# Kernel tuning notes

Hardware: AMD Instinct MI355X
Metric: run time of the kernel (lower is better)

The kernel has to match this reference:

```python
import jax, jax.numpy as jnp
import numpy as np

B, T, S, E = 32, 256, 9, 631     # batch, time, index_len, emb_num
D, FF, H, L, OUT = 512, 512, 8, 2, 512  # d_model, ffn, heads, layers, output_dim
HD = D // H
EPS = 1e-5


def _layernorm(x, g, b):
    m = jnp.mean(x, axis=-1, keepdims=True)
    v = jnp.mean(jnp.square(x - m), axis=-1, keepdims=True)
    return (x - m) * jax.lax.rsqrt(v + EPS) * g + b


def _encoder_layer(h, qkv_w, qkv_b, out_w, out_b, ln1_g, ln1_b,
                   lin1_w, lin1_b, lin2_w, lin2_b, ln2_g, ln2_b):
    # h: (N, S, D). PyTorch post-norm TransformerEncoderLayer, relu activation, dropout=0.
    N = h.shape[0]
    qkv = h @ qkv_w + qkv_b                       # (N, S, 3D)
    q, k, v = jnp.split(qkv, 3, axis=-1)
    q = q.reshape(N, S, H, HD)
    k = k.reshape(N, S, H, HD)
    v = v.reshape(N, S, H, HD)
    scores = jnp.einsum('nqhd,nkhd->nhqk', q, k) / jnp.sqrt(jnp.float32(HD))
    attn = jax.nn.softmax(scores, axis=-1)
    ctx = jnp.einsum('nhqk,nkhd->nqhd', attn, v).reshape(N, S, D)
    h = _layernorm(h + (ctx @ out_w + out_b), ln1_g, ln1_b)
    ff = jax.nn.relu(h @ lin1_w + lin1_b) @ lin2_w + lin2_b
    return _layernorm(h + ff, ln2_g, ln2_b)


def _forward(x, adapt2_w, adapt2_b, adapt_w, adapt_b,
             qkv_w, qkv_b, out_w, out_b, ln1_g, ln1_b,
             lin1_w, lin1_b, lin2_w, lin2_b, ln2_g, ln2_b, fc_w, fc_b):
    # eye_mat[x] @ W^T is a row gather: adapt_layer(onehot) == adapt_w[x] + adapt_b
    emb = adapt_w[x] + adapt_b                               # (B, T, S, D)
    # adapt_ly2(onehot.reshape(B,T,9*E)) == sum_n W2r[n, x[...,n]] + b
    w2r = adapt2_w.reshape(S, E, OUT)
    raw_emb = w2r[jnp.arange(S)[None, None, :], x].sum(axis=2) + adapt2_b  # (B, T, OUT)

    h = emb.reshape(B * T, S, D)
    for l in range(L):
        h = _encoder_layer(h, qkv_w[l], qkv_b[l], out_w[l], out_b[l],
                           ln1_g[l], ln1_b[l], lin1_w[l], lin1_b[l],
                           lin2_w[l], lin2_b[l], ln2_g[l], ln2_b[l])
    cls = h[:, 0, :]                                         # x[0] in seq-first layout
    ov = (cls @ fc_w + fc_b).reshape(B, T, OUT)
    return raw_emb * (1.0 + jax.nn.relu(ov))


def setup_inputs() -> dict:
    key = jax.random.key(0)
    ks = jax.random.split(key, 20)
    s = 0.02
    inp = {
        'x': jax.random.randint(ks[0], (B, T, S), 0, E),
        'adapt2_w': jax.random.normal(ks[1], (S * E, OUT), jnp.float32) * s,
        'adapt2_b': jnp.zeros((OUT,), jnp.float32),
        'adapt_w': jax.random.normal(ks[2], (E, D), jnp.float32) * s,
        'adapt_b': jnp.zeros((D,), jnp.float32),
        'qkv_w': jax.random.normal(ks[3], (L, D, 3 * D), jnp.float32) * s,
        'qkv_b': jnp.zeros((L, 3 * D), jnp.float32),
        'out_w': jax.random.normal(ks[4], (L, D, D), jnp.float32) * s,
        'out_b': jnp.zeros((L, D), jnp.float32),
        'ln1_g': jnp.ones((L, D), jnp.float32),
        'ln1_b': jnp.zeros((L, D), jnp.float32),
        'lin1_w': jax.random.normal(ks[5], (L, D, FF), jnp.float32) * s,
        'lin1_b': jnp.zeros((L, FF), jnp.float32),
        'lin2_w': jax.random.normal(ks[6], (L, FF, D), jnp.float32) * s,
        'lin2_b': jnp.zeros((L, D), jnp.float32),
        'ln2_g': jnp.ones((L, D), jnp.float32),
        'ln2_b': jnp.zeros((L, D), jnp.float32),
        'fc_w': jax.random.normal(ks[7], (D, OUT), jnp.float32) * s,
        'fc_b': jnp.zeros((OUT,), jnp.float32),
    }
    return inp


def reference(x, adapt2_w, adapt2_b, adapt_w, adapt_b, qkv_w, qkv_b, out_w,
              out_b, ln1_g, ln1_b, lin1_w, lin1_b, lin2_w, lin2_b, ln2_g,
              ln2_b, fc_w, fc_b):
    return _forward(x, adapt2_w, adapt2_b, adapt_w, adapt_b, qkv_w, qkv_b,
                    out_w, out_b, ln1_g, ln1_b, lin1_w, lin1_b, lin2_w,
                    lin2_b, ln2_g, ln2_b, fc_w, fc_b)
```

## Files before the change

kernel.cpp:

```cpp
#include <hip/hip_runtime.h>
#include <hip/hip_bf16.h>
#include <stdint.h>

typedef __bf16 bf16;
typedef bf16 bf16x8 __attribute__((ext_vector_type(8)));
typedef bf16 bf16x2 __attribute__((ext_vector_type(2)));
typedef float f32x4 __attribute__((ext_vector_type(4)));

__device__ __forceinline__ float b2f(bf16 x) {
  unsigned short u = __builtin_bit_cast(unsigned short, x);
  unsigned int v = ((unsigned int)u) << 16;
  return __builtin_bit_cast(float, v);
}
__device__ __forceinline__ bf16 f2b(float f) {
  unsigned int u = __builtin_bit_cast(unsigned int, f);
  unsigned int r = (u + 0x7FFFu + ((u >> 16) & 1u)) >> 16;
  return __builtin_bit_cast(bf16, (unsigned short)r);
}

__device__ __forceinline__ void async_copy16(const bf16* g, bf16* l) {
  __builtin_amdgcn_global_load_lds(
      (const __attribute__((address_space(1))) void*)g,
      (__attribute__((address_space(3))) void*)l, 16, 0, 0);
}

template <int MFR, int LDA, int LDC, int RSTR, bool RELU, bool RESID, bool RAWG, bool F32OUT, bool SWZ>
__global__ __launch_bounds__(256, (MFR == 6 ? 2 : 4)) void gemm_kernel(
    const bf16* __restrict__ A,
    const bf16* __restrict__ BT,
    const float* __restrict__ bias,
    const bf16* __restrict__ resid,
    const float* __restrict__ rawg,
    bf16* __restrict__ Cb, float* __restrict__ Cf)
{
  constexpr int K = 512;
  constexpr int MROWS = MFR * 32;
  __shared__ bf16 As[MROWS * 64];
  __shared__ bf16 Bs[128 * 64];
  const int t = threadIdx.x;
  const int lane = t & 63;
  const int wave = t >> 6;

  int bx, by;
  if (SWZ) {
    const int gn = gridDim.x, gm = gridDim.y;
    int id = blockIdx.y * gn + blockIdx.x;
    int full = (gm & ~7) * gn;
    if (id < full) {
      int sg = id / (8 * gn);
      int r = id - sg * (8 * gn);
      by = sg * 8 + (r & 7);
      bx = r >> 3;
    } else {
      int r = id - full;
      int rem = gm - (gm & ~7);
      by = (gm & ~7) + (r % rem);
      bx = r / rem;
    }
  } else {
    bx = blockIdx.x; by = blockIdx.y;
  }

  const long m0 = (long)by * MROWS;
  const int n0 = bx * 128;
  const int wm = (wave >> 1) * (MFR * 16);
  const int wn = (wave & 1) * 64;
  const int row16 = lane & 15;
  const int quad = lane >> 4;

  f32x4 acc[MFR][4] = {};

  const bf16* gA[MFR]; const bf16* gB[4];
  bf16* lA[MFR]; bf16* lB[4];
#pragma unroll
  for (int i = 0; i < MFR; i++) {
    int c = i * 256 + t;
    int row = c >> 3;
    int kc = (c & 7) ^ (row & 7);
    gA[i] = A + (m0 + row) * LDA + kc * 8;
    lA[i] = As + i * 2048 + wave * 512;
  }
#pragma unroll
  for (int i = 0; i < 4; i++) {
    int c = i * 256 + t;
    int row = c >> 3;
    int kc = (c & 7) ^ (row & 7);
    gB[i] = BT + (long)(n0 + row) * K + kc * 8;
    lB[i] = Bs + i * 2048 + wave * 512;
  }

  const int rb7 = row16 & 7;
  const bf16* paA = As + (wm + row16) * 64;
  const bf16* pbB = Bs + (wn + row16) * 64;
  const int o0 = ((0 + quad) ^ rb7) * 8;
  const int o1 = ((4 + quad) ^ rb7) * 8;

#pragma unroll 1
  for (int kt = 0; kt < K; kt += 64) {
#pragma unroll
    for (int i = 0; i < MFR; i++) async_copy16(gA[i] + kt, lA[i]);
#pragma unroll
    for (int i = 0; i < 4; i++) async_copy16(gB[i] + kt, lB[i]);
    __syncthreads();
    {
      bf16x8 af[MFR], bfr[4];
#pragma unroll
      for (int i = 0; i < MFR; i++) af[i] = *(const bf16x8*)(paA + i * 1024 + o0);
#pragma unroll
      for (int i = 0; i < 4; i++) bfr[i] = *(const bf16x8*)(pbB + i * 1024 + o0);
#pragma unroll
      for (int mi = 0; mi < MFR; mi++)
#pragma unroll
        for (int ni = 0; ni < 4; ni++)
          acc[mi][ni] = __builtin_amdgcn_mfma_f32_16x16x32_bf16(af[mi], bfr[ni], acc[mi][ni], 0, 0, 0);
    }
    {
      bf16x8 af[MFR], bfr[4];
#pragma unroll
      for (int i = 0; i < MFR; i++) af[i] = *(const bf16x8*)(paA + i * 1024 + o1);
#pragma unroll
      for (int i = 0; i < 4; i++) bfr[i] = *(const bf16x8*)(pbB + i * 1024 + o1);
#pragma unroll
      for (int mi = 0; mi < MFR; mi++)
#pragma unroll
        for (int ni = 0; ni < 4; ni++)
          acc[mi][ni] = __builtin_amdgcn_mfma_f32_16x16x32_bf16(af[mi], bfr[ni], acc[mi][ni], 0, 0, 0);
    }
    __syncthreads();
  }

  float bv[4];
#pragma unroll
  for (int ni = 0; ni < 4; ni++) bv[ni] = bias[n0 + wn + ni * 16 + row16];
#pragma unroll
  for (int mi = 0; mi < MFR; mi++) {
    long rb = m0 + wm + mi * 16 + quad * 4;
#pragma unroll
    for (int ni = 0; ni < 4; ni++) {
      int col = n0 + wn + ni * 16 + row16;
#pragma unroll
      for (int r = 0; r < 4; r++) {
        float xv = acc[mi][ni][r] + bv[ni];
        if (RESID) xv += b2f(resid[(rb + r) * RSTR + col]);
        if (RELU) xv = fmaxf(xv, 0.f);
        if (RAWG) xv = rawg[(rb + r) * 512 + col] * (1.f + fmaxf(xv, 0.f));
        if (F32OUT) Cf[(rb + r) * LDC + col] = xv;
        else        Cb[(rb + r) * LDC + col] = f2b(xv);
      }
    }
  }
}

#define ROWP 520
__global__ __launch_bounds__(512) void attn_kernel(bf16* __restrict__ qkv)
{
  __shared__ bf16 q[9 * ROWP];
  __shared__ bf16 k[9 * ROWP];
  __shared__ bf16 v[9 * ROWP];
  __shared__ float sc[8 * 81];
  const long n = blockIdx.x;
  const int t = threadIdx.x;
  bf16* base = qkv + n * (9 * 1536);
  for (int c = t; c < 1728; c += 512) {
    int o = c * 8;
    int s = o / 1536;
    int col = o - s * 1536;
    bf16x8 rawv = *(const bf16x8*)(base + o);
    bf16* dst;
    int cc;
    if (col < 512)       { dst = q; cc = col; }
    else if (col < 1024) { dst = k; cc = col - 512; }
    else                 { dst = v; cc = col - 1024; }
    *(bf16x8*)(dst + s * ROWP + cc) = rawv;
  }
  __syncthreads();
  for (int id = t; id < 648; id += 512) {
    int h = id / 81;
    int r = id - h * 81;
    int si = r / 9;
    int sj = r - si * 9;
    const bf16* qp = q + si * ROWP + h * 64;
    const bf16* kp = k + sj * ROWP + h * 64;
    float acc = 0.f;
#pragma unroll
    for (int j = 0; j < 64; j += 8) {
      bf16x8 qa = *(const bf16x8*)(qp + j);
      bf16x8 ka = *(const bf16x8*)(kp + j);
#pragma unroll
      for (int u = 0; u < 8; u++) acc += b2f(qa[u]) * b2f(ka[u]);
    }
    sc[h * 81 + si * 9 + sj] = acc * 0.125f;
  }
  __syncthreads();
  if (t < 72) {
    int h = t / 9, si = t - h * 9;
    float* row = sc + h * 81 + si * 9;
    float m = row[0];
    for (int j = 1; j < 9; j++) m = fmaxf(m, row[j]);
    float s = 0.f;
    float e[9];
    for (int j = 0; j < 9; j++) { e[j] = __expf(row[j] - m); s += e[j]; }
    float inv = 1.f / s;
    for (int j = 0; j < 9; j++) row[j] = e[j] * inv;
  }
  __syncthreads();
  for (int e2 = t; e2 < 2304; e2 += 512) {
    int si = e2 >> 8;
    int c2 = (e2 & 255) * 2;
    int h = c2 >> 6;
    const float* ar = sc + h * 81 + si * 9;
    float a0 = 0.f, a1 = 0.f;
#pragma unroll
    for (int sj = 0; sj < 9; sj++) {
      bf16x2 vv = *(const bf16x2*)(v + sj * ROWP + c2);
      float w = ar[sj];
      a0 += w * b2f(vv[0]);
      a1 += w * b2f(vv[1]);
    }
    bf16x2 o;
    o[0] = f2b(a0); o[1] = f2b(a1);
    *(bf16x2*)(base + si * 1536 + c2) = o;
  }
}

__global__ __launch_bounds__(256) void ln_kernel(const bf16* __restrict__ in, long istride,
                                                 const float* __restrict__ g, const float* __restrict__ b,
                                                 bf16* __restrict__ out, long ostride)
{
  const int t = threadIdx.x;
  const int lane = t & 63;
  const int wave = t >> 6;
  float4 g0 = *(const float4*)(g + lane * 8);
  float4 g1 = *(const float4*)(g + lane * 8 + 4);
  float4 b0 = *(const float4*)(b + lane * 8);
  float4 b1 = *(const float4*)(b + lane * 8 + 4);
  float gg[8] = {g0.x, g0.y, g0.z, g0.w, g1.x, g1.y, g1.z, g1.w};
  float bb[8] = {b0.x, b0.y, b0.z, b0.w, b1.x, b1.y, b1.z, b1.w};
#pragma unroll
  for (int r = 0; r < 2; r++) {
    const long row = ((long)blockIdx.x * 4 + wave) * 2 + r;
    const bf16* p = in + row * istride + lane * 8;
    bf16x8 xv = *(const bf16x8*)p;
    float x[8];
    float s = 0.f;
#pragma unroll
    for (int j = 0; j < 8; j++) { x[j] = b2f(xv[j]); s += x[j]; }
#pragma unroll
    for (int off = 32; off; off >>= 1) s += __shfl_xor(s, off);
    float mean = s * (1.f / 512.f);
    float vv = 0.f;
#pragma unroll
    for (int j = 0; j < 8; j++) { float d = x[j] - mean; vv += d * d; }
#pragma unroll
    for (int off = 32; off; off >>= 1) vv += __shfl_xor(vv, off);
    float inv = rsqrtf(vv * (1.f / 512.f) + 1e-5f);
    bf16x8 o;
#pragma unroll
    for (int j = 0; j < 8; j++) o[j] = f2b((x[j] - mean) * inv * gg[j] + bb[j]);
    *(bf16x8*)(out + row * ostride + lane * 8) = o;
  }
}

__global__ __launch_bounds__(256) void emb_fused_kernel(
    const int* __restrict__ x, const float* __restrict__ aw, const float* __restrict__ ab,
    bf16* __restrict__ h, int EB,
    const int* __restrict__ xs, const float* __restrict__ w2, const float* __restrict__ b2,
    float* __restrict__ raw)
{
  const int t = threadIdx.x;
  if ((int)blockIdx.x < EB) {
    const int lane = t & 63;
    const long row = (long)blockIdx.x * 4 + (t >> 6);
    const int ix = x[row];
    const float* w = aw + (long)ix * 512 + lane * 8;
    float4 w0 = *(const float4*)(w);
    float4 w1 = *(const float4*)(w + 4);
    float4 a0 = *(const float4*)(ab + lane * 8);
    float4 a1 = *(const float4*)(ab + lane * 8 + 4);
    float ww[8] = {w0.x, w0.y, w0.z, w0.w, w1.x, w1.y, w1.z, w1.w};
    float aa[8] = {a0.x, a0.y, a0.z, a0.w, a1.x, a1.y, a1.z, a1.w};
    bf16x8 o;
#pragma unroll
    for (int j = 0; j < 8; j++) o[j] = f2b(ww[j] + aa[j]);
    *(bf16x8*)(h + row * 512 + lane * 8) = o;
  } else {
    const long n = blockIdx.x - EB;
    const int c = t * 2;
    float a0 = b2[c], a1 = b2[c + 1];
    for (int s = 0; s < 9; s++) {
      int ix = xs[n * 9 + s];
      const float* p = w2 + ((long)(s * 631 + ix)) * 512 + c;
      a0 += p[0];
      a1 += p[1];
    }
    raw[n * 512 + c] = a0;
    raw[n * 512 + c + 1] = a1;
  }
}

struct TP { const float* src[9]; bf16* dst[9]; int n[9]; };
__global__ __launch_bounds__(256) void transpose_kernel(TP p)
{
  const int mid = blockIdx.z;
  const int N = p.n[mid];
  if ((int)blockIdx.x * 32 >= N) return;
  const float* src = p.src[mid];
  bf16* dst = p.dst[mid];
  __shared__ float tile[32][33];
  const int tx = threadIdx.x & 31;
  const int ty0 = (threadIdx.x >> 5) * 4;
  const long kb = (long)blockIdx.y * 32, nb = (long)blockIdx.x * 32;
#pragma unroll
  for (int i = 0; i < 4; i++) tile[ty0 + i][tx] = src[(kb + ty0 + i) * N + nb + tx];
  __syncthreads();
#pragma unroll
  for (int i = 0; i < 4; i++) dst[(nb + ty0 + i) * 512 + kb + tx] = f2b(tile[tx][ty0 + i]);
}

extern "C" void kernel_launch(void* const* d_in, const int* in_sizes, int n_in,
                              void* d_out, int out_size, void* d_ws, size_t ws_size,
                              hipStream_t stream)
{
  (void)in_sizes; (void)n_in; (void)out_size;
  const int*   x        = (const int*)d_in[0];
  const float* adapt2_w = (const float*)d_in[1];
  const float* adapt2_b = (const float*)d_in[2];
  const float* adapt_w  = (const float*)d_in[3];
  const float* adapt_b  = (const float*)d_in[4];
  const float* qkv_w    = (const float*)d_in[5];
  const float* qkv_b    = (const float*)d_in[6];
  const float* out_w    = (const float*)d_in[7];
  const float* out_b    = (const float*)d_in[8];
  const float* ln1_g    = (const float*)d_in[9];
  const float* ln1_b    = (const float*)d_in[10];
  const float* lin1_w   = (const float*)d_in[11];
  const float* lin1_b   = (const float*)d_in[12];
  const float* lin2_w   = (const float*)d_in[13];
  const float* lin2_b   = (const float*)d_in[14];
  const float* ln2_g    = (const float*)d_in[15];
  const float* ln2_b    = (const float*)d_in[16];
  const float* fc_w     = (const float*)d_in[17];
  const float* fc_b     = (const float*)d_in[18];
  float* outp = (float*)d_out;
  char* ws = (char*)d_ws;

  const long wTbytes = 6815744L;
  int G = 64;
  const int cand[7] = {1, 2, 4, 8, 16, 32, 64};
  for (int i = 0; i < 7; i++) {
    long rows = 73728L / cand[i], seqs = 8192L / cand[i];
    long need = wTbytes + rows * 1024 + rows * 3072 + seqs * 2048;
    if (need <= (long)ws_size) { G = cand[i]; break; }
  }
  const long rows_c = 73728L / G;
  const long seqs_c = 8192L / G;

  bf16*  wT    = (bf16*)(ws);
  bf16*  h_c   = (bf16*)(ws + wTbytes);
  bf16*  Qc    = (bf16*)(ws + wTbytes + rows_c * 1024);
  float* raw_c = (float*)(ws + wTbytes + rows_c * 1024 + rows_c * 3072);
  bf16* qkvT  = wT;
  bf16* outT  = wT + 1572864;
  bf16* lin1T = wT + 2097152;
  bf16* lin2T = wT + 2621440;
  bf16* fcT   = wT + 3145728;

  TP tp;
  tp.src[0] = qkv_w;           tp.dst[0] = qkvT;           tp.n[0] = 1536;
  tp.src[1] = qkv_w + 786432;  tp.dst[1] = qkvT + 786432;  tp.n[1] = 1536;
  tp.src[2] = out_w;           tp.dst[2] = outT;           tp.n[2] = 512;
  tp.src[3] = out_w + 262144;  tp.dst[3] = outT + 262144;  tp.n[3] = 512;
  tp.src[4] = lin1_w;          tp.dst[4] = lin1T;          tp.n[4] = 512;
  tp.src[5] = lin1_w + 262144; tp.dst[5] = lin1T + 262144; tp.n[5] = 512;
  tp.src[6] = lin2_w;          tp.dst[6] = lin2T;          tp.n[6] = 512;
  tp.src[7] = lin2_w + 262144; tp.dst[7] = lin2T + 262144; tp.n[7] = 512;
  tp.src[8] = fc_w;            tp.dst[8] = fcT;            tp.n[8] = 512;
  hipLaunchKernelGGL(transpose_kernel, dim3(48, 16, 9), dim3(256), 0, stream, tp);

  const bf16*  nullb = nullptr;
  const float* nullf = nullptr;
  float*       nullfo = nullptr;

  for (int g = 0; g < G; g++) {
    const long row0 = (long)g * rows_c;
    const long seq0 = (long)g * seqs_c;

    hipLaunchKernelGGL(emb_fused_kernel, dim3(rows_c / 4 + seqs_c), dim3(256), 0, stream,
        x + row0, adapt_w, adapt_b, h_c, (int)(rows_c / 4),
        x + seq0 * 9, adapt2_w, adapt2_b, raw_c);

    for (int l = 0; l < 2; l++) {
      hipLaunchKernelGGL((gemm_kernel<6, 512, 1536, 1, false, false, false, false, true>),
          dim3(12, rows_c / 192), dim3(256), 0, stream,
          h_c, qkvT + l * 786432, qkv_b + l * 1536, nullb, nullf, Qc, nullfo);
      hipLaunchKernelGGL(attn_kernel, dim3(seqs_c), dim3(512), 0, stream, Qc);
      hipLaunchKernelGGL((gemm_kernel<6, 1536, 1536, 512, false, true, false, false, true>),
          dim3(4, rows_c / 192), dim3(256), 0, stream,
          Qc, outT + l * 262144, out_b + l * 512, h_c, nullf, Qc + 1024, nullfo);
      hipLaunchKernelGGL(ln_kernel, dim3(rows_c / 8), dim3(256), 0, stream,
          Qc + 1024, 1536L, ln1_g + l * 512, ln1_b + l * 512, Qc + 512, 1536L);
      hipLaunchKernelGGL((gemm_kernel<6, 1536, 1536, 1, true, false, false, false, true>),
          dim3(4, rows_c / 192), dim3(256), 0, stream,
          Qc + 512, lin1T + l * 262144, lin1_b + l * 512, nullb, nullf, Qc, nullfo);
      hipLaunchKernelGGL((gemm_kernel<6, 1536, 512, 1536, false, true, false, false, true>),
          dim3(4, rows_c / 192), dim3(256), 0, stream,
          Qc, lin2T + l * 262144, lin2_b + l * 512, Qc + 512, nullf, h_c, nullfo);
      hipLaunchKernelGGL(ln_kernel, dim3(rows_c / 8), dim3(256), 0, stream,
          h_c, 512L, ln2_g + l * 512, ln2_b + l * 512, h_c, 512L);
    }

    hipLaunchKernelGGL((gemm_kernel<4, 4608, 512, 1, false, false, true, true, false>),
        dim3(4, seqs_c / 128), dim3(256), 0, stream,
        h_c, fcT, fc_b, nullb, raw_c, (bf16*)nullptr, outp + seq0 * 512);
  }
}
```

Before: 997.4 us.

## Load GEMM B fragments directly from global memory, shrink M tile to 128

```diff
diff --git a/kernel.cpp b/kernel.cpp
--- a/kernel.cpp
+++ b/kernel.cpp
@@ -24,8 +24,8 @@
       (__attribute__((address_space(3))) void*)l, 16, 0, 0);
 }
 
-template <int MFR, int LDA, int LDC, int RSTR, bool RELU, bool RESID, bool RAWG, bool F32OUT, bool SWZ>
-__global__ __launch_bounds__(256, (MFR == 6 ? 2 : 4)) void gemm_kernel(
+template <int LDA, int LDC, int RSTR, bool RELU, bool RESID, bool RAWG, bool F32OUT, bool SWZ>
+__global__ __launch_bounds__(256, 3) void gemm_kernel(
     const bf16* __restrict__ A,
     const bf16* __restrict__ BT,
     const float* __restrict__ bias,
@@ -34,9 +34,7 @@
     bf16* __restrict__ Cb, float* __restrict__ Cf)
 {
   constexpr int K = 512;
-  constexpr int MROWS = MFR * 32;
-  __shared__ bf16 As[MROWS * 64];
-  __shared__ bf16 Bs[128 * 64];
+  __shared__ bf16 As[128 * 64];
   const int t = threadIdx.x;
   const int lane = t & 63;
   const int wave = t >> 6;
@@ -61,71 +59,61 @@
     bx = blockIdx.x; by = blockIdx.y;
   }
 
-  const long m0 = (long)by * MROWS;
+  const long m0 = (long)by * 128;
   const int n0 = bx * 128;
-  const int wm = (wave >> 1) * (MFR * 16);
+  const int wm = (wave >> 1) * 64;
   const int wn = (wave & 1) * 64;
   const int row16 = lane & 15;
   const int quad = lane >> 4;
 
-  f32x4 acc[MFR][4] = {};
-
-  const bf16* gA[MFR]; const bf16* gB[4];
-  bf16* lA[MFR]; bf16* lB[4];
-#pragma unroll
-  for (int i = 0; i < MFR; i++) {
+  f32x4 acc[4][4] = {};
+
+  const bf16* gA[4];
+  bf16* lA[4];
+#pragma unroll
+  for (int i = 0; i < 4; i++) {
     int c = i * 256 + t;
     int row = c >> 3;
     int kc = (c & 7) ^ (row & 7);
     gA[i] = A + (m0 + row) * LDA + kc * 8;
     lA[i] = As + i * 2048 + wave * 512;
   }
-#pragma unroll
-  for (int i = 0; i < 4; i++) {
-    int c = i * 256 + t;
-    int row = c >> 3;
-    int kc = (c & 7) ^ (row & 7);
-    gB[i] = BT + (long)(n0 + row) * K + kc * 8;
-    lB[i] = Bs + i * 2048 + wave * 512;
-  }
+  const bf16* gBf[4];
+#pragma unroll
+  for (int ni = 0; ni < 4; ni++)
+    gBf[ni] = BT + (long)(n0 + wn + ni * 16 + row16) * K + quad * 8;
 
   const int rb7 = row16 & 7;
   const bf16* paA = As + (wm + row16) * 64;
-  const bf16* pbB = Bs + (wn + row16) * 64;
   const int o0 = ((0 + quad) ^ rb7) * 8;
   const int o1 = ((4 + quad) ^ rb7) * 8;
 
 #pragma unroll 1
   for (int kt = 0; kt < K; kt += 64) {
 #pragma unroll
-    for (int i = 0; i < MFR; i++) async_copy16(gA[i] + kt, lA[i]);
-#pragma unroll
-    for (int i = 0; i < 4; i++) async_copy16(gB[i] + kt, lB[i]);
+    for (int i = 0; i < 4; i++) async_copy16(gA[i] + kt, lA[i]);
+    bf16x8 b0[4];
+#pragma unroll
+    for (int ni = 0; ni < 4; ni++) b0[ni] = *(const bf16x8*)(gBf[ni] + kt);
     __syncthreads();
-    {
-      bf16x8 af[MFR], bfr[4];
-#pragma unroll
-      for (int i = 0; i < MFR; i++) af[i] = *(const bf16x8*)(paA + i * 1024 + o0);
-#pragma unroll
-      for (int i = 0; i < 4; i++) bfr[i] = *(const bf16x8*)(pbB + i * 1024 + o0);
-#pragma unroll
-      for (int mi = 0; mi < MFR; mi++)
-#pragma unroll
-        for (int ni = 0; ni < 4; ni++)
-          acc[mi][ni] = __builtin_amdgcn_mfma_f32_16x16x32_bf16(af[mi], bfr[ni], acc[mi][ni], 0, 0, 0);
-    }
-    {
-      bf16x8 af[MFR], bfr[4];
-#pragma unroll
-      for (int i = 0; i < MFR; i++) af[i] = *(const bf16x8*)(paA + i * 1024 + o1);
-#pragma unroll
-      for (int i = 0; i < 4; i++) bfr[i] = *(const bf16x8*)(pbB + i * 1024 + o1);
-#pragma unroll
-      for (int mi = 0; mi < MFR; mi++)
-#pragma unroll
-        for (int ni = 0; ni < 4; ni++)
-          acc[mi][ni] = __builtin_amdgcn_mfma_f32_16x16x32_bf16(af[mi], bfr[ni], acc[mi][ni], 0, 0, 0);
-    }
+    bf16x8 af[4];
+#pragma unroll
+    for (int i = 0; i < 4; i++) af[i] = *(const bf16x8*)(paA + i * 1024 + o0);
+    bf16x8 b1[4];
+#pragma unroll
+    for (int ni = 0; ni < 4; ni++) b1[ni] = *(const bf16x8*)(gBf[ni] + kt + 32);
+#pragma unroll
+    for (int mi = 0; mi < 4; mi++)
+#pragma unroll
+      for (int ni = 0; ni < 4; ni++)
+        acc[mi][ni] = __builtin_amdgcn_mfma_f32_16x16x32_bf16(af[mi], b0[ni], acc[mi][ni], 0, 0, 0);
+#pragma unroll
+    for (int i = 0; i < 4; i++) af[i] = *(const bf16x8*)(paA + i * 1024 + o1);
+#pragma unroll
+    for (int mi = 0; mi < 4; mi++)
+#pragma unroll
+      for (int ni = 0; ni < 4; ni++)
+        acc[mi][ni] = __builtin_amdgcn_mfma_f32_16x16x32_bf16(af[mi], b1[ni], acc[mi][ni], 0, 0, 0);
     __syncthreads();
   }
 
@@ -133,7 +121,7 @@
 #pragma unroll
   for (int ni = 0; ni < 4; ni++) bv[ni] = bias[n0 + wn + ni * 16 + row16];
 #pragma unroll
-  for (int mi = 0; mi < MFR; mi++) {
+  for (int mi = 0; mi < 4; mi++) {
     long rb = m0 + wm + mi * 16 + quad * 4;
 #pragma unroll
     for (int ni = 0; ni < 4; ni++) {
@@ -390,26 +378,26 @@
         x + seq0 * 9, adapt2_w, adapt2_b, raw_c);
 
     for (int l = 0; l < 2; l++) {
-      hipLaunchKernelGGL((gemm_kernel<6, 512, 1536, 1, false, false, false, false, true>),
-          dim3(12, rows_c / 192), dim3(256), 0, stream,
+      hipLaunchKernelGGL((gemm_kernel<512, 1536, 1, false, false, false, false, true>),
+          dim3(12, rows_c / 128), dim3(256), 0, stream,
           h_c, qkvT + l * 786432, qkv_b + l * 1536, nullb, nullf, Qc, nullfo);
       hipLaunchKernelGGL(attn_kernel, dim3(seqs_c), dim3(512), 0, stream, Qc);
-      hipLaunchKernelGGL((gemm_kernel<6, 1536, 1536, 512, false, true, false, false, true>),
-          dim3(4, rows_c / 192), dim3(256), 0, stream,
+      hipLaunchKernelGGL((gemm_kernel<1536, 1536, 512, false, true, false, false, true>),
+          dim3(4, rows_c / 128), dim3(256), 0, stream,
           Qc, outT + l * 262144, out_b + l * 512, h_c, nullf, Qc + 1024, nullfo);
       hipLaunchKernelGGL(ln_kernel, dim3(rows_c / 8), dim3(256), 0, stream,
           Qc + 1024, 1536L, ln1_g + l * 512, ln1_b + l * 512, Qc + 512, 1536L);
-      hipLaunchKernelGGL((gemm_kernel<6, 1536, 1536, 1, true, false, false, false, true>),
-          dim3(4, rows_c / 192), dim3(256), 0, stream,
+      hipLaunchKernelGGL((gemm_kernel<1536, 1536, 1, true, false, false, false, true>),
+          dim3(4, rows_c / 128), dim3(256), 0, stream,
           Qc + 512, lin1T + l * 262144, lin1_b + l * 512, nullb, nullf, Qc, nullfo);
-      hipLaunchKernelGGL((gemm_kernel<6, 1536, 512, 1536, false, true, false, false, true>),
-          dim3(4, rows_c / 192), dim3(256), 0, stream,
+      hipLaunchKernelGGL((gemm_kernel<1536, 512, 1536, false, true, false, false, true>),
+          dim3(4, rows_c / 128), dim3(256), 0, stream,
           Qc, lin2T + l * 262144, lin2_b + l * 512, Qc + 512, nullf, h_c, nullfo);
       hipLaunchKernelGGL(ln_kernel, dim3(rows_c / 8), dim3(256), 0, stream,
           h_c, 512L, ln2_g + l * 512, ln2_b + l * 512, h_c, 512L);
     }
 
-    hipLaunchKernelGGL((gemm_kernel<4, 4608, 512, 1, false, false, true, true, false>),
+    hipLaunchKernelGGL((gemm_kernel<4608, 512, 1, false, false, true, true, false>),
         dim3(4, seqs_c / 128), dim3(256), 0, stream,
         h_c, fcT, fc_b, nullb, raw_c, (bf16*)nullptr, outp + seq0 * 512);
   }
```

After: 1.553 ms. 1.56x slower.
